# Kernel optimization log

Hardware: AMD Instinct MI355X
Metric: run time of the kernel (lower is better)

The kernel has to match this reference:

```python
import jax, jax.numpy as jnp
import numpy as np

B, S, A, H1, H2, N = 32768, 512, 8, 400, 300, 3
P = 0.1          # dropout_p
NOISE_VAR = 1e-4  # _noise_variance
INV_SQRT2 = 0.7071067811865476
INV_SQRT2PI = 0.3989422804014327


def adf_relu(m, v):
    # ADF ReLU moment matching (Gast & Roth style, as in adf.ReLU)
    std = jnp.sqrt(v)
    r = m / std
    cdf = 0.5 * (1.0 + jax.lax.erf(r * INV_SQRT2))
    pdf = INV_SQRT2PI * jnp.exp(-0.5 * r * r)
    om = m * cdf + std * pdf
    ov = (m * m + v) * cdf + m * std * pdf - om * om
    return om, ov


def setup_inputs():
    key = jax.random.key(0)
    ks = jax.random.split(key, 10)
    x = jax.random.normal(ks[0], (B, S), jnp.float32)
    x_noise = jax.random.normal(ks[1], (B, S), jnp.float32)
    v1 = 10.0 / np.sqrt(S)   # fanin_init for linear1
    W1 = jax.random.uniform(ks[2], (H1, S), jnp.float32, -v1, v1)
    b1 = jax.random.uniform(ks[3], (H1,), jnp.float32, -1.0 / np.sqrt(S), 1.0 / np.sqrt(S))
    v2 = 10.0 / np.sqrt(H1)  # fanin_init for linear2
    W2 = jax.random.uniform(ks[4], (H2, H1), jnp.float32, -v2, v2)
    b2 = jax.random.uniform(ks[5], (H2,), jnp.float32, -1.0 / np.sqrt(H1), 1.0 / np.sqrt(H1))
    W3 = jax.random.uniform(ks[6], (A, H2), jnp.float32, -0.003, 0.003)
    b3 = jax.random.uniform(ks[7], (A,), jnp.float32, -0.003, 0.003)
    # MC-dropout masks for dropout_n=3 iterations, values in {0, 1/(1-p)}
    mask1 = jax.random.bernoulli(ks[8], 1.0 - P, (N, B, H1)).astype(jnp.float32) / (1.0 - P)
    mask2 = jax.random.bernoulli(ks[9], 1.0 - P, (N, B, H2)).astype(jnp.float32) / (1.0 - P)
    return dict(x=x, x_noise=x_noise, W1=W1, b1=b1, W2=W2, b2=b2, W3=W3, b3=b3,
                mask1=mask1, mask2=mask2)


def reference(x, x_noise, W1, b1, W2, b2, W3, b3, mask1, mask2):
    # input variance: _noise_variance + 2 (constant)
    var0 = jnp.full_like(x, NOISE_VAR + 2.0)
    # global min-max normalize mean, then +0.1
    mn = (x - x.min()) / (x.max() - x.min()) + 0.1
    # linear1 + ADF ReLU are deterministic: compute once, broadcast to N samples
    m = mn @ W1.T + b1              # [B,H1]
    v = var0 @ (W1 * W1).T          # [B,H1]
    m, v = adf_relu(m, v)
    m = m[None] * mask1             # [N,B,H1]
    v = v[None] * (mask1 * mask1)
    m = m @ W2.T + b2               # [N,B,H2]
    v = v @ (W2 * W2).T
    m, v = adf_relu(m, v)
    m = m * mask2
    v = v * (mask2 * mask2)
    m = m @ W3.T + b3               # [N,B,A]
    v = v @ (W3 * W3).T
    mean_out = m.mean(0)            # [B,A]
    # mean of ADF variances + empirical variance of MC means
    var_out = v.mean(0) + ((mean_out[None] - m) ** 2).mean(0)
    var_out = 10.0 ** var_out       # elementwise math.pow(10, .)
    return mean_out, var_out
```

## Files before the change

### kernel.cpp

```cpp
#include <hip/hip_runtime.h>


typedef unsigned short u16;
typedef unsigned int u32;
typedef float f32x4 __attribute__((ext_vector_type(4)));
typedef __bf16 bf16x8 __attribute__((ext_vector_type(8)));
typedef u32 u32x4 __attribute__((ext_vector_type(4)));

union U4 { u32x4 u; bf16x8 v; u16 s[8]; };

#define MFMA16(a, b, c) __builtin_amdgcn_mfma_f32_16x16x32_bf16(a, b, c, 0, 0, 0)

#define B_N 32768
#define S_N 512
#define H1_N 400
#define H2_N 300
#define A_N 8

__device__ __forceinline__ float bf2f(u16 h) {
    union { float f; u32 u; } c; c.u = ((u32)h) << 16; return c.f;
}
__device__ __forceinline__ u16 f2bfbits(float f) {
    union { __bf16 h; u16 u; } c; c.h = (__bf16)f; return c.u;
}
__device__ __forceinline__ u32 encf(float f) {
    u32 u = __float_as_uint(f);
    return (u & 0x80000000u) ? ~u : (u | 0x80000000u);
}
__device__ __forceinline__ float decf(u32 e) {
    u32 u = (e >> 31) ? (e & 0x7FFFFFFFu) : ~e;
    return __uint_as_float(u);
}

__device__ __forceinline__ void adf_relu(float m, float v, float& om, float& ov) {
    v = fmaxf(v, 1e-12f);
    float rstd = rsqrtf(v);
    float stdv = v * rstd;
    float r = m * rstd;
    float e = __expf(-0.5f * r * r);
    float ar = fabsf(r) * 0.70710678118654752f;
    float t = __builtin_amdgcn_rcpf(fmaf(0.3275911f, ar, 1.0f));
    float poly = t * (0.254829592f + t * (-0.284496736f + t * (1.421413741f +
                  t * (-1.453152027f + t * 1.061405429f))));
    float erfa = 1.0f - poly * e;
    float erfv = (r < 0.0f) ? -erfa : erfa;
    float cdf = 0.5f * (1.0f + erfv);
    float pdf = 0.3989422804014327f * e;
    om = fmaf(m, cdf, stdv * pdf);
    ov = fmaf(m * m + v, cdf, m * stdv * pdf) - om * om;
    ov = fmaxf(ov, 0.0f);
}

#define WS_CTL    0u
#define WS_B1F    64u
#define WS_B2F    1664u
#define WS_B3F    2880u
#define WS_RS1    2944u
#define WS_VC1    4544u
#define WS_W3M    6144u
#define WS_W3V    16384u
#define WS_W2SQ   26624u
#define WS_W2B    266624u
#define WS_W1B    506624u
#define WS_OMOV   916224u
#define WS_MP     53345024u
#define WS_VP     56490752u

__global__ void k_detect(const u32* __restrict__ xw, u32* __restrict__ ctl) {
    if (threadIdx.x == 0) {
        int votes = 0;
        for (int i = 0; i < 64; ++i) {
            u32 u = xw[i * 997];
            u32 e = (u >> 7) & 0xFFu;
            votes += (e >= 100u && e <= 145u) ? 1 : 0;
        }
        ctl[0] = (votes >= 40) ? 1u : 0u;
        ctl[1] = 0xFFFFFFFFu;
        ctl[2] = 0u;
    }
}

__global__ void k_weights(const void* __restrict__ w1r, const void* __restrict__ w2r,
                          const void* __restrict__ w3r, const void* __restrict__ b1r,
                          const void* __restrict__ b2r, const void* __restrict__ b3r,
                          const u32* __restrict__ ctl,
                          u16* __restrict__ w1b, u16* __restrict__ w2b,
                          u16* __restrict__ w2sq, u16* __restrict__ w3m,
                          u16* __restrict__ w3v, float* __restrict__ b1f,
                          float* __restrict__ b2f, float* __restrict__ b3f) {
    const bool bf = ctl[0] != 0u;
    const int t = blockIdx.x * 256 + threadIdx.x;

    if (t < (H2_N * H1_N / 8)) {
        float f[8];
        if (bf) {
            U4 d; d.u = *(const u32x4*)((const u16*)w2r + (size_t)t * 8);
            #pragma unroll
            for (int j = 0; j < 8; ++j) f[j] = bf2f(d.s[j]);
        } else {
            f32x4 a = *((const f32x4*)w2r + (size_t)t * 2);
            f32x4 b = *((const f32x4*)w2r + (size_t)t * 2 + 1);
            #pragma unroll
            for (int j = 0; j < 4; ++j) { f[j] = a[j]; f[4 + j] = b[j]; }
        }
        u16 sq[8], cv[8];
        #pragma unroll
        for (int j = 0; j < 8; ++j) { sq[j] = f2bfbits(f[j] * f[j]); cv[j] = f2bfbits(f[j]); }
        *(u32x4*)(w2sq + (size_t)t * 8) = *(u32x4*)sq;
        if (!bf) *(u32x4*)(w2b + (size_t)t * 8) = *(u32x4*)cv;
    }
    if (!bf && t < (H1_N * S_N / 8)) {
        f32x4 a = *((const f32x4*)w1r + (size_t)t * 2);
        f32x4 b = *((const f32x4*)w1r + (size_t)t * 2 + 1);
        u16 cv[8];
        #pragma unroll
        for (int j = 0; j < 4; ++j) { cv[j] = f2bfbits(a[j]); cv[4 + j] = f2bfbits(b[j]); }
        *(u32x4*)(w1b + (size_t)t * 8) = *(u32x4*)cv;
    }
    if (t < 16 * 320) {
        int col = t / 320, k = t - col * 320;
        float f = 0.0f;
        if (col < A_N && k < H2_N)
            f = bf ? bf2f(((const u16*)w3r)[col * H2_N + k]) : ((const float*)w3r)[col * H2_N + k];
        w3m[t] = f2bfbits(f);
        w3v[t] = f2bfbits(f * f);
    }
    if (t < H1_N) b1f[t] = bf ? bf2f(((const u16*)b1r)[t]) : ((const float*)b1r)[t];
    if (t < H2_N) b2f[t] = bf ? bf2f(((const u16*)b2r)[t]) : ((const float*)b2r)[t];
    if (t < A_N)  b3f[t] = bf ? bf2f(((const u16*)b3r)[t]) : ((const float*)b3r)[t];
}

__global__ void k_minmax(const void* __restrict__ xr, u32* __restrict__ ctl) {
    const int tid = threadIdx.x, lane = tid & 63, wv = tid >> 6;
    const bool bf = ctl[0] != 0u;
    float mn = 3.0e38f, mx = -3.0e38f;
    const int idx = blockIdx.x * 256 + tid;
    if (bf) {
        const u16* xg = (const u16*)xr;
        for (int i = idx; i < (B_N * S_N / 8); i += 2048 * 256) {
            U4 d; d.u = *(const u32x4*)(xg + (size_t)i * 8);
            #pragma unroll
            for (int j = 0; j < 8; ++j) {
                float f = bf2f(d.s[j]);
                mn = fminf(mn, f); mx = fmaxf(mx, f);
            }
        }
    } else {
        const f32x4* xf = (const f32x4*)xr;
        for (int i = idx; i < (B_N * S_N / 4); i += 2048 * 256) {
            f32x4 d = xf[i];
            #pragma unroll
            for (int j = 0; j < 4; ++j) {
                mn = fminf(mn, d[j]); mx = fmaxf(mx, d[j]);
            }
        }
    }
    #pragma unroll
    for (int off = 32; off >= 1; off >>= 1) {
        mn = fminf(mn, __shfl_xor(mn, off));
        mx = fmaxf(mx, __shfl_xor(mx, off));
    }
    __shared__ float rmn[4], rmx[4];
    if (lane == 0) { rmn[wv] = mn; rmx[wv] = mx; }
    __syncthreads();
    if (tid == 0) {
        for (int w = 1; w < 4; ++w) { mn = fminf(mn, rmn[w]); mx = fmaxf(mx, rmx[w]); }
        atomicMin(&ctl[1], encf(mn));
        atomicMax(&ctl[2], encf(mx));
    }
}

__global__ void k_prep(const void* __restrict__ w1r, const u32* __restrict__ ctl,
                       float* __restrict__ rs1, float* __restrict__ vc1) {
    const bool bf = ctl[0] != 0u;
    const int h = blockIdx.x, lane = threadIdx.x;
    float f[8];
    if (bf) {
        U4 d; d.u = *(const u32x4*)((const u16*)w1r + (size_t)h * S_N + lane * 8);
        #pragma unroll
        for (int j = 0; j < 8; ++j) f[j] = bf2f(d.s[j]);
    } else {
        f32x4 a = *((const f32x4*)w1r + (size_t)h * 128 + lane * 2);
        f32x4 b = *((const f32x4*)w1r + (size_t)h * 128 + lane * 2 + 1);
        #pragma unroll
        for (int j = 0; j < 4; ++j) { f[j] = a[j]; f[4 + j] = b[j]; }
    }
    float s1 = 0.f, s2 = 0.f;
    #pragma unroll
    for (int j = 0; j < 8; ++j) { s1 += f[j]; s2 += f[j] * f[j]; }
    #pragma unroll
    for (int off = 32; off >= 1; off >>= 1) {
        s1 += __shfl_xor(s1, off);
        s2 += __shfl_xor(s2, off);
    }
    if (lane == 0) { rs1[h] = s1; vc1[h] = 2.0001f * s2; }
}

__global__ __launch_bounds__(256, 4)
void k_l1(const void* __restrict__ xr, const u16* __restrict__ w1bf,
          const u16* __restrict__ w1cv, const float* __restrict__ b1f,
          const float* __restrict__ rs1, const float* __restrict__ vc1,
          const u32* __restrict__ ctl, u32* __restrict__ omovg) {
    const int tid = threadIdx.x, wv = tid >> 6, lane = tid & 63;
    const int lrow = lane & 15, lgrp = lane >> 4;
    const int m0 = blockIdx.y * 128;
    const int n0 = blockIdx.x * 112;
    const bool bf = ctl[0] != 0u;
    const u16* w1 = bf ? w1bf : w1cv;
    const float xmin = decf(ctl[1]), xmax = decf(ctl[2]);
    const float inv = 1.0f / (xmax - xmin);
    const float csh = 0.1f - xmin * inv;

    const f32x4 fz = {0.f, 0.f, 0.f, 0.f};
    f32x4 acc[2][7];
    #pragma unroll
    for (int i = 0; i < 2; ++i)
        #pragma unroll
        for (int j = 0; j < 7; ++j) acc[i][j] = fz;

    const int rowA = m0 + wv * 32 + lrow;
    if (bf) {
        const u16* xg = (const u16*)xr;
        const size_t ar0 = (size_t)rowA * S_N + lgrp * 8;
        const size_t ar1 = ar0 + (size_t)16 * S_N;
        U4 nx0, nx1;
        nx0.u = *(const u32x4*)(xg + ar0);
        nx1.u = *(const u32x4*)(xg + ar1);
        for (int ks = 0; ks < 16; ++ks) {
            U4 a0 = nx0, a1 = nx1;
            if (ks < 15) {
                nx0.u = *(const u32x4*)(xg + ar0 + (ks + 1) * 32);
                nx1.u = *(const u32x4*)(xg + ar1 + (ks + 1) * 32);
            }
            const int k = ks * 32 + lgrp * 8;
            #pragma unroll
            for (int ct = 0; ct < 7; ++ct) {
                const int col = n0 + ct * 16 + lrow;
                U4 b; b.u = 0;
                if (col < H1_N) b.u = *(const u32x4*)(w1 + (size_t)col * S_N + k);
                acc[0][ct] = MFMA16(a0.v, b.v, acc[0][ct]);
                acc[1][ct] = MFMA16(a1.v, b.v, acc[1][ct]);
            }
        }
    } else {
        const f32x4* xf = (const f32x4*)xr;
        const size_t q0 = ((size_t)rowA * S_N + lgrp * 8) >> 2;
        const size_t q1 = q0 + (size_t)16 * S_N / 4;
        f32x4 n0a = xf[q0], n0b = xf[q0 + 1], n1a = xf[q1], n1b = xf[q1 + 1];
        for (int ks = 0; ks < 16; ++ks) {
            f32x4 c0a = n0a, c0b = n0b, c1a = n1a, c1b = n1b;
            if (ks < 15) {
                const size_t o = (size_t)(ks + 1) * 8;
                n0a = xf[q0 + o]; n0b = xf[q0 + o + 1];
                n1a = xf[q1 + o]; n1b = xf[q1 + o + 1];
            }
            U4 a0, a1;
            #pragma unroll
            for (int j = 0; j < 4; ++j) {
                a0.s[j] = f2bfbits(c0a[j]); a0.s[4 + j] = f2bfbits(c0b[j]);
                a1.s[j] = f2bfbits(c1a[j]); a1.s[4 + j] = f2bfbits(c1b[j]);
            }
            const int k = ks * 32 + lgrp * 8;
            #pragma unroll
            for (int ct = 0; ct < 7; ++ct) {
                const int col = n0 + ct * 16 + lrow;
                U4 b; b.u = 0;
                if (col < H1_N) b.u = *(const u32x4*)(w1 + (size_t)col * S_N + k);
                acc[0][ct] = MFMA16(a0.v, b.v, acc[0][ct]);
                acc[1][ct] = MFMA16(a1.v, b.v, acc[1][ct]);
            }
        }
    }
    #pragma unroll
    for (int ct = 0; ct < 7; ++ct) {
        const int col = n0 + ct * 16 + lrow;
        if (col < H1_N) {
            const float c1 = csh * rs1[col] + b1f[col];
            const float vv = vc1[col];
            #pragma unroll
            for (int r2 = 0; r2 < 2; ++r2)
                #pragma unroll
                for (int r = 0; r < 4; ++r) {
                    const int row = m0 + wv * 32 + r2 * 16 + lgrp * 4 + r;
                    float mm = fmaf(inv, acc[r2][ct][r], c1);
                    float omx, ovx; adf_relu(mm, vv, omx, ovx);
                    omovg[(size_t)row * H1_N + col] =
                        (u32)f2bfbits(omx) | ((u32)f2bfbits(ovx) << 16);
                }
        }
    }
}

__global__ __launch_bounds__(256, 3)
void k_l23(const u32* __restrict__ omovg, const u16* __restrict__ w2bf,
           const u16* __restrict__ w2cv, const u16* __restrict__ w2sqg,
           const void* __restrict__ m1r, const void* __restrict__ m2r,
           const float* __restrict__ b2f,
           const u16* __restrict__ w3mg, const u16* __restrict__ w3vg,
           const u32* __restrict__ ctl, float* __restrict__ mpart,
           float* __restrict__ vpart) {
    __shared__ __align__(16) unsigned char smem[52224];
    u16* pmS = (u16*)smem;
    u16* pvS = (u16*)(smem + 26112);
    u16* m2s = (u16*)smem;
    u16* v2s = (u16*)(smem + 26112);

    const int tid = threadIdx.x;
    const int wv = tid >> 6, lane = tid & 63;
    const int lrow = lane & 15, lgrp = lane >> 4;
    const int bx = blockIdx.x;
    const int n = bx % 3;
    const int m0 = (bx / 3) * 32;
    const bool bf = ctl[0] != 0u;
    const u16* w2 = bf ? w2bf : w2cv;
    const f32x4 fz = {0.f, 0.f, 0.f, 0.f};

    #pragma unroll 2
    for (int p = 0; p < 7; ++p) {
        const int c = tid + p * 256;
        if (c < 1600) {
            const int row = c / 50, kc = (c - row * 50) * 8;
            const size_t base = (size_t)(m0 + row) * H1_N + kc;
            u32x4 o0 = *(const u32x4*)(omovg + base);
            u32x4 o1 = *(const u32x4*)(omovg + base + 4);
            const size_t mb = ((size_t)n * B_N + m0 + row) * H1_N + kc;
            u32x4 k0 = {0, 0, 0, 0}, k1 = {0, 0, 0, 0};
            if (bf) {
                k0 = *(const u32x4*)((const u16*)m1r + mb);
            } else {
                k0 = *(const u32x4*)((const float*)m1r + mb);
                k1 = *(const u32x4*)((const float*)m1r + mb + 4);
            }
            u16 pm[8], pv[8];
            #pragma unroll
            for (int j = 0; j < 8; ++j) {
                const u32 w = (j < 4) ? o0[j] : o1[j - 4];
                const float omf = __uint_as_float(w << 16);
                const float ovf = __uint_as_float(w & 0xFFFF0000u);
                float mf;
                if (bf) {
                    const u32 mw = k0[j >> 1];
                    mf = bf2f((u16)((j & 1) ? (mw >> 16) : (mw & 0xFFFFu)));
                } else {
                    mf = __uint_as_float((j < 4) ? k0[j] : k1[j - 4]);
                }
                pm[j] = f2bfbits(omf * mf);
                pv[j] = f2bfbits(ovf * mf * mf);
            }
            *(u32x4*)(pmS + row * 408 + kc) = *(u32x4*)pm;
            *(u32x4*)(pvS + row * 408 + kc) = *(u32x4*)pv;
        }
    }
    __syncthreads();

    f32x4 accM[2][5], accV[2][5];
    #pragma unroll
    for (int i = 0; i < 2; ++i)
        #pragma unroll
        for (int j = 0; j < 5; ++j) { accM[i][j] = fz; accV[i][j] = fz; }

    #pragma unroll 1
    for (int ks = 0; ks < 12; ++ks) {
        const int k0 = ks * 32;
        bf16x8 amf[2], avf[2];
        #pragma unroll
        for (int r2 = 0; r2 < 2; ++r2) {
            const int idx = (r2 * 16 + lrow) * 408 + k0 + lgrp * 8;
            amf[r2] = *(const bf16x8*)(pmS + idx);
            avf[r2] = *(const bf16x8*)(pvS + idx);
        }
        const int kb = k0 + lgrp * 8;
        #pragma unroll
        for (int ct = 0; ct < 5; ++ct) {
            const int col = wv * 80 + ct * 16 + lrow;
            U4 bm, bv; bm.u = 0; bv.u = 0;
            if (col < H2_N) {
                const size_t bidx = (size_t)col * H1_N + kb;
                bm.u = *(const u32x4*)(w2 + bidx);
                bv.u = *(const u32x4*)(w2sqg + bidx);
            }
            accM[0][ct] = MFMA16(amf[0], bm.v, accM[0][ct]);
            accM[1][ct] = MFMA16(amf[1], bm.v, accM[1][ct]);
            accV[0][ct] = MFMA16(avf[0], bv.v, accV[0][ct]);
            accV[1][ct] = MFMA16(avf[1], bv.v, accV[1][ct]);
        }
    }
    {
        const bool kv = lgrp < 2;
        const int ko = kv ? lgrp * 8 : 0;
        bf16x8 amf[2], avf[2];
        #pragma unroll
        for (int r2 = 0; r2 < 2; ++r2) {
            const int idx = (r2 * 16 + lrow) * 408 + 384 + ko;
            U4 ta, tv;
            ta.v = *(const bf16x8*)(pmS + idx);
            tv.v = *(const bf16x8*)(pvS + idx);
            if (!kv) { ta.u = 0; tv.u = 0; }
            amf[r2] = ta.v; avf[r2] = tv.v;
        }
        const int kb = 384 + lgrp * 8;
        #pragma unroll
        for (int ct = 0; ct < 5; ++ct) {
            const int col = wv * 80 + ct * 16 + lrow;
            U4 bm, bv; bm.u = 0; bv.u = 0;
            if (col < H2_N && kb < H1_N) {
                const size_t bidx = (size_t)col * H1_N + kb;
                bm.u = *(const u32x4*)(w2 + bidx);
                bv.u = *(const u32x4*)(w2sqg + bidx);
            }
            accM[0][ct] = MFMA16(amf[0], bm.v, accM[0][ct]);
            accM[1][ct] = MFMA16(amf[1], bm.v, accM[1][ct]);
            accV[0][ct] = MFMA16(avf[0], bv.v, accV[0][ct]);
            accV[1][ct] = MFMA16(avf[1], bv.v, accV[1][ct]);
        }
    }
    __syncthreads();

    float msk[2][5][4];
    #pragma unroll
    for (int r2 = 0; r2 < 2; ++r2)
        #pragma unroll
        for (int ct = 0; ct < 5; ++ct) {
            const int col = wv * 80 + ct * 16 + lrow;
            #pragma unroll
            for (int r = 0; r < 4; ++r) {
                const int rl = r2 * 16 + lgrp * 4 + r;
                float mf = 0.0f;
                if (col < H2_N) {
                    const size_t midx = ((size_t)n * B_N + m0 + rl) * H2_N + col;
                    mf = bf ? bf2f(((const u16*)m2r)[midx])
                            : ((const float*)m2r)[midx];
                }
                msk[r2][ct][r] = mf;
            }
        }

    #pragma unroll
    for (int r2 = 0; r2 < 2; ++r2)
        #pragma unroll
        for (int ct = 0; ct < 5; ++ct) {
            const int col = wv * 80 + ct * 16 + lrow;
            const float b2v = (col < H2_N) ? b2f[col] : 0.0f;
            #pragma unroll
            for (int r = 0; r < 4; ++r) {
                const int rl = r2 * 16 + lgrp * 4 + r;
                u16 wm = 0, wvs = 0;
                if (col < H2_N) {
                    float mm = accM[r2][ct][r] + b2v;
                    float vvx = accV[r2][ct][r];
                    float omx, ovx; adf_relu(mm, vvx, omx, ovx);
                    const float mskv = msk[r2][ct][r];
                    wm  = f2bfbits(omx * mskv);
                    wvs = f2bfbits(ovx * mskv * mskv);
                }
                m2s[rl * 328 + col] = wm;
                v2s[rl * 328 + col] = wvs;
            }
        }
    __syncthreads();

    {
        const int typ = wv & 1, rt = wv >> 1;
        const u16* slab = typ ? v2s : m2s;
        const u16* w3t  = typ ? w3vg : w3mg;
        f32x4 c3 = fz;
        #pragma unroll
        for (int kk = 0; kk < 10; ++kk) {
            const int aidx = (rt * 16 + lrow) * 328 + kk * 32 + lgrp * 8;
            bf16x8 af = *(const bf16x8*)(slab + aidx);
            U4 bw; bw.u = *(const u32x4*)(w3t + (size_t)lrow * 320 + kk * 32 + lgrp * 8);
            c3 = MFMA16(af, bw.v, c3);
        }
        float* part = typ ? vpart : mpart;
        if (lrow < A_N) {
            #pragma unroll
            for (int r = 0; r < 4; ++r) {
                const int rl = rt * 16 + lgrp * 4 + r;
                part[((size_t)n * B_N + m0 + rl) * 8 + lrow] = c3[r];
            }
        }
    }
}

__global__ __launch_bounds__(256)
void k_out(const float* __restrict__ mpart, const float* __restrict__ vpart,
           const float* __restrict__ b3f, const u32* __restrict__ ctl,
           void* __restrict__ outr) {
    const size_t idx = (size_t)blockIdx.x * 256 + threadIdx.x;
    const int a = (int)(idx & 7);
    const size_t st = (size_t)B_N * 8;
    const float m0 = mpart[idx], m1 = mpart[st + idx], m2 = mpart[2 * st + idx];
    const float v0 = vpart[idx], v1 = vpart[st + idx], v2 = vpart[2 * st + idx];
    const float md = (m0 + m1 + m2) * (1.0f / 3.0f);
    const float sm2 = (m0 * m0 + m1 * m1 + m2 * m2) * (1.0f / 3.0f);
    const float meanout = md + b3f[a];
    const float vexp = (v0 + v1 + v2) * (1.0f / 3.0f) + sm2 - md * md;
    const float varout = __expf(vexp * 2.302585092994046f);
    const bool bf = ctl[0] != 0u;
    if (bf) {
        ((u16*)outr)[idx] = f2bfbits(meanout);
        ((u16*)outr)[st + idx] = f2bfbits(varout);
    } else {
        ((float*)outr)[idx] = meanout;
        ((float*)outr)[st + idx] = varout;
    }
}

extern "C" void kernel_launch(void* const* d_in, const int* in_sizes, int n_in,
                              void* d_out, int out_size, void* d_ws, size_t ws_size,
                              hipStream_t stream) {
    const void* x     = d_in[0];
    const void* W1    = d_in[2];
    const void* b1    = d_in[3];
    const void* W2    = d_in[4];
    const void* b2    = d_in[5];
    const void* W3    = d_in[6];
    const void* b3    = d_in[7];
    const void* mask1 = d_in[8];
    const void* mask2 = d_in[9];

    char* ws = (char*)d_ws;
    u32*   ctl   = (u32*)(ws + WS_CTL);
    float* b1f   = (float*)(ws + WS_B1F);
    float* b2f   = (float*)(ws + WS_B2F);
    float* b3f   = (float*)(ws + WS_B3F);
    float* rs1   = (float*)(ws + WS_RS1);
    float* vc1   = (float*)(ws + WS_VC1);
    u16*   w3m   = (u16*)(ws + WS_W3M);
    u16*   w3v   = (u16*)(ws + WS_W3V);
    u16*   w2sq  = (u16*)(ws + WS_W2SQ);
    u16*   w2b   = (u16*)(ws + WS_W2B);
    u16*   w1b   = (u16*)(ws + WS_W1B);
    u32*   omov  = (u32*)(ws + WS_OMOV);
    float* mpart = (float*)(ws + WS_MP);
    float* vpart = (float*)(ws + WS_VP);

    k_detect<<<1, 64, 0, stream>>>((const u32*)x, ctl);
    k_weights<<<100, 256, 0, stream>>>(W1, W2, W3, b1, b2, b3, ctl,
                                       w1b, w2b, w2sq, w3m, w3v, b1f, b2f, b3f);
    k_minmax<<<2048, 256, 0, stream>>>(x, ctl);
    k_prep<<<400, 64, 0, stream>>>(W1, ctl, rs1, vc1);
    k_l1<<<dim3(4, 256), 256, 0, stream>>>(x, (const u16*)W1, w1b, b1f, rs1, vc1,
                                           ctl, omov);
    k_l23<<<3072, 256, 0, stream>>>(omov, (const u16*)W2, w2b, w2sq, mask1, mask2,
                                    b2f, w3m, w3v, ctl, mpart, vpart);
    k_out<<<1024, 256, 0, stream>>>(mpart, vpart, b3f, ctl, d_out);
}
```

Baseline: 666.7 us.

## Fuse layer-1 GEMM and ADF ReLU into the layer-2/3 kernel

Removes the separate layer-1 kernel and its packed mean/variance intermediate buffer; each layer-2/3 block now computes layer 1 for its 32 rows across all 400 hidden units and writes masked results straight into shared memory. This eliminates a large global write/read round trip and a kernel launch. In exchange, layer 1 is recomputed once per dropout sample (3x), every block streams the full W1 matrix, and mask1 loads become scalar instead of vectorized.

Result: slower. 827.5 us (+24.1%).

```diff
diff --git a/kernel.cpp b/kernel.cpp
--- a/kernel.cpp
+++ b/kernel.cpp
@@ -62,7 +62,6 @@
 #define WS_W2SQ   26624u
 #define WS_W2B    266624u
 #define WS_W1B    506624u
-#define WS_OMOV   916224u
 #define WS_MP     53345024u
 #define WS_VP     56490752u
 
@@ -196,29 +195,46 @@
     if (lane == 0) { rs1[h] = s1; vc1[h] = 2.0001f * s2; }
 }
 
-__global__ __launch_bounds__(256, 4)
-void k_l1(const void* __restrict__ xr, const u16* __restrict__ w1bf,
-          const u16* __restrict__ w1cv, const float* __restrict__ b1f,
-          const float* __restrict__ rs1, const float* __restrict__ vc1,
-          const u32* __restrict__ ctl, u32* __restrict__ omovg) {
-    const int tid = threadIdx.x, wv = tid >> 6, lane = tid & 63;
+__global__ __launch_bounds__(256, 3)
+void k_l23f(const void* __restrict__ xr, const u16* __restrict__ w1bf,
+            const u16* __restrict__ w1cv, const float* __restrict__ b1f,
+            const float* __restrict__ rs1, const float* __restrict__ vc1,
+            const u16* __restrict__ w2bf, const u16* __restrict__ w2cv,
+            const u16* __restrict__ w2sqg,
+            const void* __restrict__ m1r, const void* __restrict__ m2r,
+            const float* __restrict__ b2f,
+            const u16* __restrict__ w3mg, const u16* __restrict__ w3vg,
+            const u32* __restrict__ ctl, float* __restrict__ mpart,
+            float* __restrict__ vpart) {
+    __shared__ __align__(16) unsigned char smem[52224];
+    u16* pmS = (u16*)smem;
+    u16* pvS = (u16*)(smem + 26112);
+    u16* m2s = (u16*)smem;
+    u16* v2s = (u16*)(smem + 26112);
+
+    const int tid = threadIdx.x;
+    const int wv = tid >> 6, lane = tid & 63;
     const int lrow = lane & 15, lgrp = lane >> 4;
-    const int m0 = blockIdx.y * 128;
-    const int n0 = blockIdx.x * 112;
+    const int bx = blockIdx.x;
+    const int n = bx % 3;
+    const int m0 = (bx / 3) * 32;
     const bool bf = ctl[0] != 0u;
     const u16* w1 = bf ? w1bf : w1cv;
+    const u16* w2 = bf ? w2bf : w2cv;
+    const f32x4 fz = {0.f, 0.f, 0.f, 0.f};
     const float xmin = decf(ctl[1]), xmax = decf(ctl[2]);
     const float inv = 1.0f / (xmax - xmin);
     const float csh = 0.1f - xmin * inv;
 
-    const f32x4 fz = {0.f, 0.f, 0.f, 0.f};
-    f32x4 acc[2][7];
+    const int cntw  = wv ? 6 : 7;
+    const int cbase = wv ? (16 + 96 * wv) : 0;
+    f32x4 acc1[2][7];
     #pragma unroll
     for (int i = 0; i < 2; ++i)
         #pragma unroll
-        for (int j = 0; j < 7; ++j) acc[i][j] = fz;
-
-    const int rowA = m0 + wv * 32 + lrow;
+        for (int j = 0; j < 7; ++j) acc1[i][j] = fz;
+
+    const int rowA = m0 + lrow;
     if (bf) {
         const u16* xg = (const u16*)xr;
         const size_t ar0 = (size_t)rowA * S_N + lgrp * 8;
@@ -235,11 +251,12 @@
             const int k = ks * 32 + lgrp * 8;
             #pragma unroll
             for (int ct = 0; ct < 7; ++ct) {
-                const int col = n0 + ct * 16 + lrow;
-                U4 b; b.u = 0;
-                if (col < H1_N) b.u = *(const u32x4*)(w1 + (size_t)col * S_N + k);
-                acc[0][ct] = MFMA16(a0.v, b.v, acc[0][ct]);
-                acc[1][ct] = MFMA16(a1.v, b.v, acc[1][ct]);
+                if (ct < cntw) {
+                    const int col = cbase + ct * 16 + lrow;
+                    U4 b; b.u = *(const u32x4*)(w1 + (size_t)col * S_N + k);
+                    acc1[0][ct] = MFMA16(a0.v, b.v, acc1[0][ct]);
+                    acc1[1][ct] = MFMA16(a1.v, b.v, acc1[1][ct]);
+                }
             }
         }
     } else {
@@ -263,92 +280,35 @@
             const int k = ks * 32 + lgrp * 8;
             #pragma unroll
             for (int ct = 0; ct < 7; ++ct) {
-                const int col = n0 + ct * 16 + lrow;
-                U4 b; b.u = 0;
-                if (col < H1_N) b.u = *(const u32x4*)(w1 + (size_t)col * S_N + k);
-                acc[0][ct] = MFMA16(a0.v, b.v, acc[0][ct]);
-                acc[1][ct] = MFMA16(a1.v, b.v, acc[1][ct]);
-            }
-        }
-    }
+                if (ct < cntw) {
+                    const int col = cbase + ct * 16 + lrow;
+                    U4 b; b.u = *(const u32x4*)(w1 + (size_t)col * S_N + k);
+                    acc1[0][ct] = MFMA16(a0.v, b.v, acc1[0][ct]);
+                    acc1[1][ct] = MFMA16(a1.v, b.v, acc1[1][ct]);
+                }
+            }
+        }
+    }
+
     #pragma unroll
     for (int ct = 0; ct < 7; ++ct) {
-        const int col = n0 + ct * 16 + lrow;
-        if (col < H1_N) {
+        if (ct < cntw) {
+            const int col = cbase + ct * 16 + lrow;
             const float c1 = csh * rs1[col] + b1f[col];
             const float vv = vc1[col];
             #pragma unroll
             for (int r2 = 0; r2 < 2; ++r2)
                 #pragma unroll
                 for (int r = 0; r < 4; ++r) {
-                    const int row = m0 + wv * 32 + r2 * 16 + lgrp * 4 + r;
-                    float mm = fmaf(inv, acc[r2][ct][r], c1);
+                    const int rl = r2 * 16 + lgrp * 4 + r;
+                    float mm = fmaf(inv, acc1[r2][ct][r], c1);
                     float omx, ovx; adf_relu(mm, vv, omx, ovx);
-                    omovg[(size_t)row * H1_N + col] =
-                        (u32)f2bfbits(omx) | ((u32)f2bfbits(ovx) << 16);
+                    const size_t midx = ((size_t)n * B_N + m0 + rl) * H1_N + col;
+                    const float mf = bf ? bf2f(((const u16*)m1r)[midx])
+                                        : ((const float*)m1r)[midx];
+                    pmS[rl * 408 + col] = f2bfbits(omx * mf);
+                    pvS[rl * 408 + col] = f2bfbits(ovx * mf * mf);
                 }
-        }
-    }
-}
-
-__global__ __launch_bounds__(256, 3)
-void k_l23(const u32* __restrict__ omovg, const u16* __restrict__ w2bf,
-           const u16* __restrict__ w2cv, const u16* __restrict__ w2sqg,
-           const void* __restrict__ m1r, const void* __restrict__ m2r,
-           const float* __restrict__ b2f,
-           const u16* __restrict__ w3mg, const u16* __restrict__ w3vg,
-           const u32* __restrict__ ctl, float* __restrict__ mpart,
-           float* __restrict__ vpart) {
-    __shared__ __align__(16) unsigned char smem[52224];
-    u16* pmS = (u16*)smem;
-    u16* pvS = (u16*)(smem + 26112);
-    u16* m2s = (u16*)smem;
-    u16* v2s = (u16*)(smem + 26112);
-
-    const int tid = threadIdx.x;
-    const int wv = tid >> 6, lane = tid & 63;
-    const int lrow = lane & 15, lgrp = lane >> 4;
-    const int bx = blockIdx.x;
-    const int n = bx % 3;
-    const int m0 = (bx / 3) * 32;
-    const bool bf = ctl[0] != 0u;
-    const u16* w2 = bf ? w2bf : w2cv;
-    const f32x4 fz = {0.f, 0.f, 0.f, 0.f};
-
-    #pragma unroll 2
-    for (int p = 0; p < 7; ++p) {
-        const int c = tid + p * 256;
-        if (c < 1600) {
-            const int row = c / 50, kc = (c - row * 50) * 8;
-            const size_t base = (size_t)(m0 + row) * H1_N + kc;
-            u32x4 o0 = *(const u32x4*)(omovg + base);
-            u32x4 o1 = *(const u32x4*)(omovg + base + 4);
-            const size_t mb = ((size_t)n * B_N + m0 + row) * H1_N + kc;
-            u32x4 k0 = {0, 0, 0, 0}, k1 = {0, 0, 0, 0};
-            if (bf) {
-                k0 = *(const u32x4*)((const u16*)m1r + mb);
-            } else {
-                k0 = *(const u32x4*)((const float*)m1r + mb);
-                k1 = *(const u32x4*)((const float*)m1r + mb + 4);
-            }
-            u16 pm[8], pv[8];
-            #pragma unroll
-            for (int j = 0; j < 8; ++j) {
-                const u32 w = (j < 4) ? o0[j] : o1[j - 4];
-                const float omf = __uint_as_float(w << 16);
-                const float ovf = __uint_as_float(w & 0xFFFF0000u);
-                float mf;
-                if (bf) {
-                    const u32 mw = k0[j >> 1];
-                    mf = bf2f((u16)((j & 1) ? (mw >> 16) : (mw & 0xFFFFu)));
-                } else {
-                    mf = __uint_as_float((j < 4) ? k0[j] : k1[j - 4]);
-                }
-                pm[j] = f2bfbits(omf * mf);
-                pv[j] = f2bfbits(ovf * mf * mf);
-            }
-            *(u32x4*)(pmS + row * 408 + kc) = *(u32x4*)pm;
-            *(u32x4*)(pvS + row * 408 + kc) = *(u32x4*)pv;
         }
     }
     __syncthreads();
@@ -531,7 +491,6 @@
     u16*   w2sq  = (u16*)(ws + WS_W2SQ);
     u16*   w2b   = (u16*)(ws + WS_W2B);
     u16*   w1b   = (u16*)(ws + WS_W1B);
-    u32*   omov  = (u32*)(ws + WS_OMOV);
     float* mpart = (float*)(ws + WS_MP);
     float* vpart = (float*)(ws + WS_VP);
 
@@ -540,9 +499,8 @@
                                        w1b, w2b, w2sq, w3m, w3v, b1f, b2f, b3f);
     k_minmax<<<2048, 256, 0, stream>>>(x, ctl);
     k_prep<<<400, 64, 0, stream>>>(W1, ctl, rs1, vc1);
-    k_l1<<<dim3(4, 256), 256, 0, stream>>>(x, (const u16*)W1, w1b, b1f, rs1, vc1,
-                                           ctl, omov);
-    k_l23<<<3072, 256, 0, stream>>>(omov, (const u16*)W2, w2b, w2sq, mask1, mask2,
-                                    b2f, w3m, w3v, ctl, mpart, vpart);
+    k_l23f<<<3072, 256, 0, stream>>>(x, (const u16*)W1, w1b, b1f, rs1, vc1,
+                                     (const u16*)W2, w2b, w2sq, mask1, mask2,
+                                     b2f, w3m, w3v, ctl, mpart, vpart);
     k_out<<<1024, 256, 0, stream>>>(mpart, vpart, b3f, ctl, d_out);
 }
```
